# Kernel tuning notes

Measured on AMD Instinct MI355X. Metric: run time of the kernel, lower is better.

## Reference

```python
import jax, jax.numpy as jnp
import numpy as np

CONF_T = 0.05
IOU_T = 0.5
K_PER_CLASS = 200  # max_detections_per_class
MAX_DET = 200      # max_detections
VAR = jnp.array([0.1, 0.1, 0.2, 0.2], jnp.float32)


def setup_inputs() -> dict:
    key = jax.random.key(0)
    k1, k2, k3, k4 = jax.random.split(key, 4)
    B, A, C = 8, 76725, 80
    # logits shifted down so most sigmoid scores fall below threshold (realistic)
    head_classifier = jax.random.normal(k1, (B, A, C), jnp.float32) - 2.0
    head_regression = jax.random.normal(k2, (B, A, 4), jnp.float32)
    centers = jax.random.uniform(k3, (A, 2), jnp.float32, 0.0, 640.0)
    sizes = jax.random.uniform(k4, (A, 2), jnp.float32, 16.0, 256.0)
    anchor_boxes = jnp.concatenate([centers, sizes], axis=-1)  # (cx, cy, w, h)
    return {"head_classifier": head_classifier,
            "head_regression": head_regression,
            "anchor_boxes": anchor_boxes}


def _decode(anchors, box_pred):
    # anchors: [1, A, 4] (cx,cy,w,h); box_pred: [B, A, 4]
    b = box_pred * VAR
    cxcy = b[..., :2] * anchors[..., 2:] + anchors[..., :2]
    wh = jnp.exp(b[..., 2:]) * anchors[..., 2:]
    # center -> corner coordinates (x1, y1, x2, y2)
    return jnp.concatenate([cxcy - wh * 0.5, cxcy + wh * 0.5], axis=-1)


def _pairwise_iou(bx):
    # bx: [K, 4] corner boxes -> [K, K] IoU
    x1, y1, x2, y2 = jnp.split(bx, 4, axis=-1)  # each [K, 1]
    area = jnp.squeeze((x2 - x1) * (y2 - y1), -1)  # [K]
    ix1 = jnp.maximum(x1, x1.T)
    iy1 = jnp.maximum(y1, y1.T)
    ix2 = jnp.minimum(x2, x2.T)
    iy2 = jnp.minimum(y2, y2.T)
    inter = jnp.clip(ix2 - ix1, 0.0) * jnp.clip(iy2 - iy1, 0.0)  # [K, K]
    union = area[:, None] + area[None, :] - inter
    return inter / jnp.maximum(union, 1e-8)


def _nms_one_class(scores, boxes):
    # scores: [A], boxes: [A, 4] -> top-K greedy NMS
    vals, idx = jax.lax.top_k(scores, K_PER_CLASS)
    b = boxes[idx]  # [K, 4]
    valid = vals > CONF_T
    iou = _pairwise_iou(b)  # [K, K]
    order = jnp.arange(K_PER_CLASS)

    def body(i, keep):
        # if box i is kept, suppress later boxes overlapping it above IOU_T
        sup = (iou[i] > IOU_T) & (order > i) & keep[i]
        return keep & ~sup

    keep = jax.lax.fori_loop(0, K_PER_CLASS, body, valid)
    return jnp.where(keep, vals, -1.0), b


def _combined(cls_scores, boxes):
    # cls_scores: [A, C], boxes: [A, 4] (shared across classes, q=1)
    sc, bx = jax.vmap(lambda s: _nms_one_class(s, boxes), in_axes=1)(cls_scores)
    C = sc.shape[0]
    cls_ids = jnp.broadcast_to(
        jnp.arange(C, dtype=jnp.float32)[:, None], (C, K_PER_CLASS))
    sc_f = sc.reshape(-1)          # [C*K]
    bx_f = bx.reshape(-1, 4)       # [C*K, 4]
    cl_f = cls_ids.reshape(-1)     # [C*K]
    top_v, top_i = jax.lax.top_k(sc_f, MAX_DET)
    ok = top_v > 0.0  # surviving detections (kept scores exceed CONF_T > 0)
    nmsed_boxes = jnp.where(ok[:, None], bx_f[top_i], 0.0)
    nmsed_scores = jnp.where(ok, top_v, 0.0)
    nmsed_classes = jnp.where(ok, cl_f[top_i], 0.0)
    valid = jnp.sum(ok).astype(jnp.int32)
    return nmsed_boxes, nmsed_scores, nmsed_classes, valid


def reference(head_classifier, head_regression, anchor_boxes):
    cls_predictions = jax.nn.sigmoid(head_classifier)          # [B, A, C]
    boxes = _decode(anchor_boxes[None, ...], head_regression)  # [B, A, 4]
    return jax.vmap(_combined)(cls_predictions, boxes)
```

## Files before the change

### kernel.cpp

```cpp
#include <hip/hip_runtime.h>
#include <cstdint>

#define TPB 256

constexpr int B_ = 8;
constexpr int A_ = 76725;
constexpr int C_ = 80;
constexpr int K_ = 200;
constexpr int CAP = 1024;
constexpr int LCAP = 16;
constexpr int NBC = B_ * C_;
constexpr int P_ = 16;
constexpr int SL_ = C_ * K_ / P_;
constexpr float T0 = 0.4f;
constexpr float CONF_Tf = 0.05f;
constexpr float IOU_Tf = 0.5f;

__device__ inline uint64_t pack_key(float v, unsigned idx) {
  unsigned u = __float_as_uint(v);
  u = (u & 0x80000000u) ? ~u : (u | 0x80000000u);
  return ((uint64_t)u << 32) | (uint64_t)(0xFFFFFFFFu ^ idx);
}
__device__ inline float key_val(uint64_t k) {
  unsigned u = (unsigned)(k >> 32);
  u = (u & 0x80000000u) ? (u & 0x7FFFFFFFu) : ~u;
  return __uint_as_float(u);
}
__device__ inline unsigned key_idx(uint64_t k) { return 0xFFFFFFFFu ^ (unsigned)k; }

__device__ void radix_select(uint64_t* act, uint64_t* nxt, int n, int R,
                             uint64_t* sel, int* scnt, unsigned* hist,
                             int* s_d, int* s_ncnt) {
  int tid = threadIdx.x;
  if (tid == 0) *scnt = 0;
  __syncthreads();
  if (n <= R) {
    for (int i = tid; i < n; i += TPB) sel[i] = act[i];
    if (tid == 0) *scnt = n;
    __syncthreads();
    return;
  }
  int w = tid >> 6;
  for (int shift = 56; shift >= 0; shift -= 8) {
    for (int i = tid; i < 4 * 256; i += TPB) hist[i] = 0;
    __syncthreads();
    for (int i = tid; i < n; i += TPB)
      atomicAdd(&hist[(w << 8) + (int)((act[i] >> shift) & 255)], 1u);
    __syncthreads();
    if (tid < 256)
      hist[tid] = hist[tid] + hist[256 + tid] + hist[512 + tid] + hist[768 + tid];
    __syncthreads();
    for (int off = 1; off < 256; off <<= 1) {
      unsigned add = (tid < 256 && tid + off < 256) ? hist[tid + off] : 0u;
      __syncthreads();
      if (tid < 256) hist[tid] += add;
      __syncthreads();
    }
    if (tid < 256) {
      unsigned s = hist[tid];
      unsigned s1 = (tid == 255) ? 0u : hist[tid + 1];
      if ((int)s >= R && (int)s1 < R) *s_d = tid;
    }
    if (tid == 0) *s_ncnt = 0;
    __syncthreads();
    int d = *s_d;
    int above = (d == 255) ? 0 : (int)hist[d + 1];
    int cntd = (int)hist[d] - above;
    int need = R - above;
    if (need == cntd) {
      for (int i = tid; i < n; i += TPB)
        if ((int)((act[i] >> shift) & 255) >= d) sel[atomicAdd(scnt, 1)] = act[i];
      __syncthreads();
      return;
    }
    if (cntd == n) { R = need; continue; }
    for (int i = tid; i < n; i += TPB) {
      int dg = (int)((act[i] >> shift) & 255);
      if (dg > d) sel[atomicAdd(scnt, 1)] = act[i];
      else if (dg == d) nxt[atomicAdd(s_ncnt, 1)] = act[i];
    }
    __syncthreads();
    uint64_t* t = act; act = nxt; nxt = t;
    n = cntd; R = need;
  }
  for (int i = tid; i < R && i < n; i += TPB) sel[atomicAdd(scnt, 1)] = act[i];
  __syncthreads();
}

__device__ inline uint64_t shfl_xor_u64(uint64_t x, int m) {
  unsigned lo = (unsigned)__shfl_xor((int)(unsigned)x, m, 64);
  unsigned hi = (unsigned)__shfl_xor((int)(x >> 32), m, 64);
  return ((uint64_t)hi << 32) | lo;
}
__device__ void sort256_desc(uint64_t* sel) {
  int tid = threadIdx.x;
  uint64_t v = sel[tid];
  for (int k = 2; k <= 256; k <<= 1) {
    for (int j = k >> 1; j > 0; j >>= 1) {
      uint64_t other;
      if (j >= 64) {
        sel[tid] = v;
        __syncthreads();
        other = sel[tid ^ j];
        __syncthreads();
      } else {
        other = shfl_xor_u64(v, j);
      }
      bool up = ((tid & k) == 0);
      bool lower = ((tid & j) == 0);
      bool takeMax = (up == lower);
      bool sw = takeMax ? (other > v) : (other < v);
      v = sw ? other : v;
    }
  }
  sel[tid] = v;
  __syncthreads();
}

__device__ inline void bitonic_sort_desc_1024(uint64_t* buf, int tid) {
  for (int k = 2; k <= 1024; k <<= 1) {
    for (int j = k >> 1; j > 0; j >>= 1) {
      for (int i = tid; i < 1024; i += TPB) {
        int ixj = i ^ j;
        if (ixj > i) {
          uint64_t a = buf[i], b = buf[ixj];
          bool dir = ((i & k) == 0);
          if ((a < b) == dir) { buf[i] = b; buf[ixj] = a; }
        }
      }
      __syncthreads();
    }
  }
}
__device__ inline void compact_topk(uint64_t* buf, int* s_cnt, float* s_thr, int tid) {
  int cnt = *s_cnt;
  if (cnt > 1024) cnt = 1024;
  for (int i = cnt + tid; i < 1024; i += TPB) buf[i] = 0;
  __syncthreads();
  bitonic_sort_desc_1024(buf, tid);
  if (tid == 0) {
    *s_cnt = cnt < K_ ? cnt : K_;
    if (cnt >= K_) *s_thr = key_val(buf[K_ - 1]);
  }
  __syncthreads();
}
template <typename F>
__device__ inline void stream_topk(int n, F fetch, uint64_t* buf, int* s_cnt,
                                   float* s_thr, int tid) {
  for (int base = 0; base < n; base += TPB) {
    int i = base + tid;
    if (i < n) {
      uint64_t key; float v;
      fetch(i, key, v);
      if (v >= *s_thr) {
        int p = atomicAdd(s_cnt, 1);
        if (p < 1024) buf[p] = key;
      }
    }
    __syncthreads();
    int cur = *s_cnt;
    __syncthreads();
    if (cur >= 768) compact_topk(buf, s_cnt, s_thr, tid);
  }
  compact_topk(buf, s_cnt, s_thr, tid);
}

__global__ __launch_bounds__(TPB) void candidates_kernel(const float* __restrict__ logits,
                                                         uint64_t* __restrict__ lists,
                                                         int* __restrict__ cnts) {
  __shared__ uint64_t s_cand[C_][LCAP];
  __shared__ int s_cnt[C_];
  constexpr int ANCH = 256;
  constexpr int nT = (A_ + ANCH - 1) / ANCH;
  int bb = blockIdx.x / nT, t = blockIdx.x - bb * nT;
  int a0 = t * ANCH;
  int na = min(ANCH, A_ - a0);
  int tid = threadIdx.x;
  for (int c = tid; c < C_; c += TPB) s_cnt[c] = 0;
  __syncthreads();

  const float4* src = (const float4*)(logits + ((size_t)bb * A_ + (size_t)a0) * C_);
  const int nq = na * (C_ / 4);
  for (int q0 = tid; q0 < nq; q0 += TPB * 4) {
    float4 v[4];
    int qv[4] = {q0, q0 + TPB, q0 + 2 * TPB, q0 + 3 * TPB};
#pragma unroll
    for (int u = 0; u < 4; ++u)
      if (qv[u] < nq) v[u] = src[qv[u]];
#pragma unroll
    for (int u = 0; u < 4; ++u) {
      int q = qv[u];
      if (q >= nq) continue;
      float lv[4] = {v[u].x, v[u].y, v[u].z, v[u].w};
      int pos = q * 4;
      int al = pos / C_;
      int c  = pos - al * C_;
#pragma unroll
      for (int j = 0; j < 4; ++j) {
        float l = lv[j];
        if (l > T0) {
          float s = 1.0f / (1.0f + expf(-l));
          uint64_t key = pack_key(s, (unsigned)(a0 + al));
          int p = atomicAdd(&s_cnt[c + j], 1);
          if (p < LCAP) {
            s_cand[c + j][p] = key;
          } else {
            int cc = bb * C_ + c + j;
            int g = atomicAdd(&cnts[cc * 16], 1);
            if (g < CAP) lists[(size_t)cc * CAP + g] = key;
          }
        }
      }
    }
  }
  __syncthreads();

  if (tid < C_) {
    int n = min(s_cnt[tid], LCAP);
    if (n > 0) {
      int cc = bb * C_ + tid;
      int base = atomicAdd(&cnts[cc * 16], n);
      uint64_t* dst = lists + (size_t)cc * CAP;
      for (int j = 0; j < n; ++j) {
        int p = base + j;
        if (p < CAP) dst[p] = s_cand[tid][j];
      }
    }
  }
}

__global__ __launch_bounds__(TPB) void class_nms_kernel(const float* __restrict__ logits,
                                                        const float4* __restrict__ regs,
                                                        const float4* __restrict__ anchors,
                                                        const uint64_t* __restrict__ lists,
                                                        const int* __restrict__ cnts,
                                                        float* __restrict__ cls_scores,
                                                        float4* __restrict__ cls_boxes) {
  __shared__ uint64_t s_bufA[1024];
  __shared__ uint64_t s_bufB[1024];
  __shared__ uint64_t s_sel[256];
  __shared__ unsigned s_hist[4 * 256];
  __shared__ int s_scnt, s_d, s_ncnt;
  __shared__ int s_cnt;
  __shared__ float s_thr;
  __shared__ float4 s_box[K_];
  __shared__ float s_score[K_], s_area[K_];
  __shared__ unsigned long long s_mask[K_][4];
  __shared__ unsigned long long s_keep[4];

  int tid = threadIdx.x;
  int cc = blockIdx.x;
  int bb = cc / C_, c = cc - bb * C_;
  int total = cnts[cc * 16];
  int m;

  if (total >= K_ && total <= CAP) {
    const uint64_t* lp = lists + (size_t)cc * CAP;
    for (int i = tid; i < total; i += TPB) s_bufA[i] = lp[i];
    __syncthreads();
    radix_select(s_bufA, s_bufB, total, K_, s_sel, &s_scnt, s_hist, &s_d, &s_ncnt);
    m = K_;
    if (tid >= m) s_sel[tid] = 0;
    __syncthreads();
    sort256_desc(s_sel);
  } else {
    if (tid == 0) { s_cnt = 0; s_thr = CONF_Tf; }
    __syncthreads();
    const float* col = logits + (size_t)bb * A_ * C_ + c;
    stream_topk(A_,
        [&](int i, uint64_t& key, float& v) {
          float l = col[(size_t)i * C_];
          v = 1.0f / (1.0f + expf(-l));
          key = pack_key(v, (unsigned)i);
        },
        s_bufA, &s_cnt, &s_thr, tid);
    m = s_cnt;
    s_sel[tid] = (tid < m) ? s_bufA[tid] : 0;
    __syncthreads();
  }

  if (tid < K_) {
    if (tid < m) {
      uint64_t key = s_sel[tid];
      unsigned a = key_idx(key);
      float4 r = regs[(size_t)bb * A_ + a];
      float4 an = anchors[a];
      float bxv = __fmul_rn(r.x, 0.1f), byv = __fmul_rn(r.y, 0.1f);
      float bwv = __fmul_rn(r.z, 0.2f), bhv = __fmul_rn(r.w, 0.2f);
      float cx = __fadd_rn(__fmul_rn(bxv, an.z), an.x);
      float cy = __fadd_rn(__fmul_rn(byv, an.w), an.y);
      float w  = __fmul_rn(expf(bwv), an.z);
      float h  = __fmul_rn(expf(bhv), an.w);
      float hw = __fmul_rn(w, 0.5f), hh = __fmul_rn(h, 0.5f);
      float4 bx = make_float4(__fsub_rn(cx, hw), __fsub_rn(cy, hh),
                              __fadd_rn(cx, hw), __fadd_rn(cy, hh));
      s_score[tid] = key_val(key);
      s_box[tid] = bx;
      s_area[tid] = __fmul_rn(__fsub_rn(bx.z, bx.x), __fsub_rn(bx.w, bx.y));
    } else {
      s_score[tid] = -1.0f;
      s_box[tid] = make_float4(0.f, 0.f, 0.f, 0.f);
      s_area[tid] = 0.f;
    }
  }
  __syncthreads();

  if (tid < K_) {
    float4 bk = s_box[tid];
    float ak = s_area[tid];
    unsigned long long mw[4] = {0ull, 0ull, 0ull, 0ull};
    for (int i = 0; i < tid; ++i) {
      float4 bi = s_box[i];
      float ix1 = fmaxf(bk.x, bi.x), iy1 = fmaxf(bk.y, bi.y);
      float ix2 = fminf(bk.z, bi.z), iy2 = fminf(bk.w, bi.w);
      float iw = fmaxf(__fsub_rn(ix2, ix1), 0.f);
      float ih = fmaxf(__fsub_rn(iy2, iy1), 0.f);
      float inter = __fmul_rn(iw, ih);
      float uni = __fsub_rn(__fadd_rn(ak, s_area[i]), inter);
      float iou = inter / fmaxf(uni, 1e-8f);
      if (iou > IOU_Tf) mw[i >> 6] |= (1ull << (i & 63));
    }
    s_mask[tid][0] = mw[0]; s_mask[tid][1] = mw[1];
    s_mask[tid][2] = mw[2]; s_mask[tid][3] = mw[3];
  }
  __syncthreads();

  if (tid == 0) {
    unsigned long long k0 = 0, k1 = 0, k2 = 0, k3 = 0;
    for (int i = 0; i < m; ++i) {
      if (s_score[i] > CONF_Tf) {
        bool sup = ((s_mask[i][0] & k0) | (s_mask[i][1] & k1) |
                    (s_mask[i][2] & k2) | (s_mask[i][3] & k3)) != 0ull;
        if (!sup) {
          if (i < 64)       k0 |= 1ull << i;
          else if (i < 128) k1 |= 1ull << (i - 64);
          else if (i < 192) k2 |= 1ull << (i - 128);
          else              k3 |= 1ull << (i - 192);
        }
      }
    }
    s_keep[0] = k0; s_keep[1] = k1; s_keep[2] = k2; s_keep[3] = k3;
  }
  __syncthreads();

  if (tid < K_) {
    bool kept = (tid < m) && ((s_keep[tid >> 6] >> (tid & 63)) & 1ull);
    size_t o = (size_t)cc * K_ + tid;
    cls_scores[o] = kept ? s_score[tid] : -1.0f;
    cls_boxes[o] = s_box[tid];
  }
}

__global__ __launch_bounds__(TPB) void part_topk_kernel(const float* __restrict__ cls_scores,
                                                        uint64_t* __restrict__ tmp) {
  __shared__ uint64_t bufA[SL_];
  __shared__ uint64_t bufB[SL_];
  __shared__ uint64_t sel[256];
  __shared__ unsigned hist[4 * 256];
  __shared__ int s_scnt, s_d, s_ncnt;
  int tid = threadIdx.x;
  int bb = blockIdx.x / P_, part = blockIdx.x - bb * P_;
  int f0 = part * SL_;
  const float* sc = cls_scores + (size_t)bb * C_ * K_ + f0;
  for (int i = tid; i < SL_; i += TPB) bufA[i] = pack_key(sc[i], (unsigned)(f0 + i));
  __syncthreads();
  radix_select(bufA, bufB, SL_, K_, sel, &s_scnt, hist, &s_d, &s_ncnt);
  if (tid < K_) tmp[(size_t)blockIdx.x * K_ + tid] = sel[tid];
}

__global__ __launch_bounds__(TPB) void final_topk_kernel(const float4* __restrict__ cls_boxes,
                                                         const uint64_t* __restrict__ tmp,
                                                         float* __restrict__ out) {
  constexpr int NF = P_ * K_;
  __shared__ uint64_t bufA[NF];
  __shared__ uint64_t bufB[NF];
  __shared__ uint64_t sel[256];
  __shared__ unsigned hist[4 * 256];
  __shared__ int s_scnt, s_d, s_ncnt, s_m;
  int tid = threadIdx.x;
  int bb = blockIdx.x;
  const uint64_t* tp = tmp + (size_t)bb * NF;
  for (int i = tid; i < NF; i += TPB) bufA[i] = tp[i];
  __syncthreads();
  radix_select(bufA, bufB, NF, K_, sel, &s_scnt, hist, &s_d, &s_ncnt);
  if (tid >= s_scnt) sel[tid] = 0;
  if (tid == 0) s_m = K_;
  __syncthreads();
  sort256_desc(sel);
  if (tid < K_) {
    float v = key_val(sel[tid]);
    if (!(v > 0.0f)) atomicMin(&s_m, tid);
  }
  __syncthreads();
  int m = s_m;

  if (tid < K_) {
    float4 bx = make_float4(0.f, 0.f, 0.f, 0.f);
    float sv = 0.f, cv = 0.f;
    if (tid < m) {
      uint64_t key = sel[tid];
      unsigned f = key_idx(key);
      sv = key_val(key);
      cv = (float)(f / K_);
      bx = cls_boxes[(size_t)bb * C_ * K_ + f];
    }
    ((float4*)out)[(size_t)bb * K_ + tid] = bx;
    out[B_ * K_ * 4 + bb * K_ + tid] = sv;
    out[B_ * K_ * 5 + bb * K_ + tid] = cv;
  }
  if (tid == 0) out[B_ * K_ * 6 + bb] = (float)m;
}

extern "C" void kernel_launch(void* const* d_in, const int* in_sizes, int n_in,
                              void* d_out, int out_size, void* d_ws, size_t ws_size,
                              hipStream_t stream) {
  const float* logits  = (const float*)d_in[0];
  const float4* regs   = (const float4*)d_in[1];
  const float4* anchors = (const float4*)d_in[2];
  float* out = (float*)d_out;

  char* ws = (char*)d_ws;
  uint64_t* lists    = (uint64_t*)ws;              size_t off = (size_t)NBC * CAP * 8;
  int* cnts          = (int*)(ws + off);           off += (size_t)NBC * 16 * 4;
  float* cls_scores  = (float*)(ws + off);         off += (size_t)NBC * K_ * 4;
  float4* cls_boxes  = (float4*)(ws + off);        off += (size_t)NBC * K_ * 16;
  uint64_t* tmp      = (uint64_t*)(ws + off);

  hipMemsetAsync(cnts, 0, (size_t)NBC * 16 * 4, stream);
  constexpr int nT = (A_ + 255) / 256;
  candidates_kernel<<<B_ * nT, TPB, 0, stream>>>(logits, lists, cnts);
  class_nms_kernel<<<NBC, TPB, 0, stream>>>(logits, regs, anchors, lists, cnts,
                                            cls_scores, cls_boxes);
  part_topk_kernel<<<B_ * P_, TPB, 0, stream>>>(cls_scores, tmp);
  final_topk_kernel<<<B_, TPB, 0, stream>>>(cls_boxes, tmp, out);
}
```

Baseline: 410.2 us.

## Balance IoU mask work across threads and deepen candidate load unroll

Replaces the triangular per-thread IoU loop, where thread k handled k pairs, with a flat distribution of all K*(K-1)/2 pairs across threads. Each pair index is mapped to (k,i) with a sqrt inverse and the suppression bit is set by a shared-memory atomicOr. This removes the load imbalance in which the last threads did about 200 iterations while others idled. It also precomputes the confidence mask with a ballot for the serial greedy loop, and unrolls the candidate scan's loads from 4 to 8 float4 per thread to raise memory-level parallelism, at the cost of more registers.

```diff
diff --git a/kernel.cpp b/kernel.cpp
--- a/kernel.cpp
+++ b/kernel.cpp
@@ -181,14 +181,16 @@
 
   const float4* src = (const float4*)(logits + ((size_t)bb * A_ + (size_t)a0) * C_);
   const int nq = na * (C_ / 4);
-  for (int q0 = tid; q0 < nq; q0 += TPB * 4) {
-    float4 v[4];
-    int qv[4] = {q0, q0 + TPB, q0 + 2 * TPB, q0 + 3 * TPB};
+  for (int q0 = tid; q0 < nq; q0 += TPB * 8) {
+    float4 v[8];
+    int qv[8];
 #pragma unroll
-    for (int u = 0; u < 4; ++u)
+    for (int u = 0; u < 8; ++u) {
+      qv[u] = q0 + u * TPB;
       if (qv[u] < nq) v[u] = src[qv[u]];
+    }
 #pragma unroll
-    for (int u = 0; u < 4; ++u) {
+    for (int u = 0; u < 8; ++u) {
       int q = qv[u];
       if (q >= nq) continue;
       float lv[4] = {v[u].x, v[u].y, v[u].z, v[u].w};
@@ -247,6 +249,7 @@
   __shared__ float s_score[K_], s_area[K_];
   __shared__ unsigned long long s_mask[K_][4];
   __shared__ unsigned long long s_keep[4];
+  __shared__ unsigned long long s_conf[4];
 
   int tid = threadIdx.x;
   int cc = blockIdx.x;
@@ -303,32 +306,35 @@
       s_area[tid] = 0.f;
     }
   }
-  __syncthreads();
-
-  if (tid < K_) {
-    float4 bk = s_box[tid];
-    float ak = s_area[tid];
-    unsigned long long mw[4] = {0ull, 0ull, 0ull, 0ull};
-    for (int i = 0; i < tid; ++i) {
-      float4 bi = s_box[i];
-      float ix1 = fmaxf(bk.x, bi.x), iy1 = fmaxf(bk.y, bi.y);
-      float ix2 = fminf(bk.z, bi.z), iy2 = fminf(bk.w, bi.w);
-      float iw = fmaxf(__fsub_rn(ix2, ix1), 0.f);
-      float ih = fmaxf(__fsub_rn(iy2, iy1), 0.f);
-      float inter = __fmul_rn(iw, ih);
-      float uni = __fsub_rn(__fadd_rn(ak, s_area[i]), inter);
-      float iou = inter / fmaxf(uni, 1e-8f);
-      if (iou > IOU_Tf) mw[i >> 6] |= (1ull << (i & 63));
-    }
-    s_mask[tid][0] = mw[0]; s_mask[tid][1] = mw[1];
-    s_mask[tid][2] = mw[2]; s_mask[tid][3] = mw[3];
+  for (int i = tid; i < K_ * 4; i += TPB) ((unsigned long long*)s_mask)[i] = 0ull;
+  __syncthreads();
+  unsigned long long bal = __ballot(tid < K_ && s_score[tid] > CONF_Tf);
+  if ((tid & 63) == 0) s_conf[tid >> 6] = bal;
+
+  constexpr int NP = K_ * (K_ - 1) / 2;
+  for (int p = tid; p < NP; p += TPB) {
+    int k = (int)((1.0f + sqrtf(1.0f + 8.0f * (float)p)) * 0.5f);
+    while (k * (k - 1) / 2 > p) --k;
+    while (k * (k + 1) / 2 <= p) ++k;
+    int i = p - k * (k - 1) / 2;
+    float4 bk = s_box[k], bi = s_box[i];
+    float ix1 = fmaxf(bk.x, bi.x), iy1 = fmaxf(bk.y, bi.y);
+    float ix2 = fminf(bk.z, bi.z), iy2 = fminf(bk.w, bi.w);
+    float iw = fmaxf(__fsub_rn(ix2, ix1), 0.f);
+    float ih = fmaxf(__fsub_rn(iy2, iy1), 0.f);
+    float inter = __fmul_rn(iw, ih);
+    float uni = __fsub_rn(__fadd_rn(s_area[k], s_area[i]), inter);
+    float iou = inter / fmaxf(uni, 1e-8f);
+    if (iou > IOU_Tf) atomicOr(&s_mask[k][i >> 6], 1ull << (i & 63));
   }
   __syncthreads();
 
   if (tid == 0) {
     unsigned long long k0 = 0, k1 = 0, k2 = 0, k3 = 0;
+    unsigned long long c0 = s_conf[0], c1 = s_conf[1], c2 = s_conf[2], c3 = s_conf[3];
     for (int i = 0; i < m; ++i) {
-      if (s_score[i] > CONF_Tf) {
+      unsigned long long cw = (i < 64) ? c0 : (i < 128) ? c1 : (i < 192) ? c2 : c3;
+      if ((cw >> (i & 63)) & 1ull) {
         bool sup = ((s_mask[i][0] & k0) | (s_mask[i][1] & k1) |
                     (s_mask[i][2] & k2) | (s_mask[i][3] & k3)) != 0ull;
         if (!sup) {
```

Measured after the change: 425.5 us. 3.7% more time.
